# Optimization experiments

Hardware: AMD Instinct MI355X
Metric: run time of the kernel (lower is better)

## Reference

```python
import jax, jax.numpy as jnp
import numpy as np

N_NODES = 50000
N_EDGES = 800000
IN_SIZE = 128
NUM_HEADS = 8
HEAD_DIM = IN_SIZE // NUM_HEADS  # qk/val head dim = 16


def setup_inputs() -> dict:
    key = jax.random.key(0)
    ks = jax.random.split(key, 16)
    d = IN_SIZE
    lim = 1.0 / np.sqrt(d)
    inp = {
        "in_feats": jax.random.normal(ks[0], (N_NODES, d), jnp.float32),
        "struc_feats": jax.random.normal(ks[1], (N_NODES, d), jnp.float32),
        "edge_weights": jax.random.uniform(ks[2], (N_EDGES,), jnp.float32),
        "ln_scale": jnp.ones((d,), jnp.float32),
        "ln_bias": jnp.zeros((d,), jnp.float32),
        "Ws": jax.random.uniform(ks[3], (d, d), jnp.float32, -lim, lim),
        "bs": jnp.zeros((d,), jnp.float32),
        "Wq": jax.random.uniform(ks[4], (d, d), jnp.float32, -lim, lim),
        "bq": jnp.zeros((d,), jnp.float32),
        "Wk": jax.random.uniform(ks[5], (d, d), jnp.float32, -lim, lim),
        "bk": jnp.zeros((d,), jnp.float32),
        "Wv": jax.random.uniform(ks[6], (d, d), jnp.float32, -lim, lim),
        "bv": jnp.zeros((d,), jnp.float32),
        "Wo": jax.random.uniform(ks[7], (d, d), jnp.float32, -lim, lim),
        "edge_ids": jax.random.randint(ks[8], (2, N_EDGES), 0, N_NODES, jnp.int64)
        if jax.config.jax_enable_x64 else jax.random.randint(ks[8], (2, N_EDGES), 0, N_NODES, jnp.int32),
    }
    return inp


def _layer_norm(x, scale, bias, eps=1e-5):
    mu = jnp.mean(x, axis=-1, keepdims=True)
    var = jnp.var(x, axis=-1, keepdims=True)
    return (x - mu) * jax.lax.rsqrt(var + eps) * scale + bias


def reference(in_feats, struc_feats, edge_weights, ln_scale, ln_bias,
              Ws, bs, Wq, bq, Wk, bk, Wv, bv, Wo, edge_ids):
    N = in_feats.shape[0]
    H, hd = NUM_HEADS, HEAD_DIM

    delta = _layer_norm(in_feats, ln_scale, ln_bias)           # pre-norm
    delta = jax.nn.gelu(delta, approximate=False)               # pre-activation (exact GELU, torch default)
    delta_struc = delta + struc_feats @ Ws.T + bs               # struc_proj add

    qry = (delta_struc @ Wq.T + bq) / np.sqrt(hd)                # [N, qk]
    keyf = delta_struc @ Wk.T + bk                               # [N, qk]
    val = delta @ Wv.T + bv                                      # [N, val]

    src, dst = edge_ids[0], edge_ids[1]                          # out[src] += A[src,dst] * val[dst]
    qe = qry[src].reshape(-1, H, hd)                             # [E, H, hd]
    ke = keyf[dst].reshape(-1, H, hd)                            # [E, H, hd]
    attn = jax.nn.sigmoid(jnp.sum(qe * ke, axis=-1))             # [E, H]
    attn = edge_weights[:, None] * attn

    msgs = attn[:, :, None] * val[dst].reshape(-1, H, hd)        # [E, H, hd]
    agg = jax.ops.segment_sum(msgs.reshape(-1, H * hd), src, num_segments=N)  # [N, val]

    out = agg @ Wo.T                                             # out_proj (no bias)
    return in_feats + out                                        # skip connection
```

## Files before the change

### kernel.cpp

```cpp
#include <hip/hip_runtime.h>
#include <math.h>

#define NF 128

typedef __attribute__((ext_vector_type(8))) short short8;
typedef __attribute__((ext_vector_type(4))) float floatx4;

__device__ __forceinline__ unsigned short f2bf(float f) {
    union { float x; unsigned int i; } c; c.x = f;
    unsigned int r = c.i + 0x7fffu + ((c.i >> 16) & 1u);
    return (unsigned short)(r >> 16);
}
__device__ __forceinline__ float bf2f(unsigned short u) {
    union { unsigned int i; float x; } c; c.i = ((unsigned int)u) << 16;
    return c.x;
}
__device__ __forceinline__ void unpack8(uint4 u, float* f) {
    union { unsigned int i; float x; } c;
    c.i = u.x << 16;          f[0] = c.x;
    c.i = u.x & 0xffff0000u;  f[1] = c.x;
    c.i = u.y << 16;          f[2] = c.x;
    c.i = u.y & 0xffff0000u;  f[3] = c.x;
    c.i = u.z << 16;          f[4] = c.x;
    c.i = u.z & 0xffff0000u;  f[5] = c.x;
    c.i = u.w << 16;          f[6] = c.x;
    c.i = u.w & 0xffff0000u;  f[7] = c.x;
}
__device__ __forceinline__ ushort4 pack4(float a, float b, float c, float d) {
    ushort4 h; h.x = f2bf(a); h.y = f2bf(b); h.z = f2bf(c); h.w = f2bf(d);
    return h;
}

__global__ __launch_bounds__(256) void wconv5z_kernel(
    const float* __restrict__ a, const float* __restrict__ b,
    const float* __restrict__ c, const float* __restrict__ d,
    const float* __restrict__ e, unsigned short* __restrict__ o,
    int* __restrict__ cnt, int N)
{
    int blk = blockIdx.x;
    if (blk < 320) {
        int i = blk * 256 + threadIdx.x;
        int w = i >> 14, j = i & 16383;
        const float* p = (w == 0) ? a : (w == 1) ? b : (w == 2) ? c : (w == 3) ? d : e;
        o[i] = f2bf(p[j]);
    } else {
        int i = (blk - 320) * 256 + threadIdx.x;
        if (i < N) cnt[i] = 0;
    }
}

__global__ __launch_bounds__(256) void ln_kernel(
    const float* __restrict__ in_feats, const float* __restrict__ gamma,
    const float* __restrict__ beta, unsigned short* __restrict__ deltab, int M)
{
    int gi = blockIdx.x * 256 + threadIdx.x;
    int row = gi >> 2, t4 = gi & 3;
    if (row >= M) return;
    size_t rbase = (size_t)row * NF;

    const float4* ip = (const float4*)(in_feats + rbase) + t4 * 8;
    float4 xf[8];
    #pragma unroll
    for (int p = 0; p < 8; ++p) xf[p] = ip[p];
    float s = 0.f, sq = 0.f;
    #pragma unroll
    for (int p = 0; p < 8; ++p) {
        s  += xf[p].x + xf[p].y + xf[p].z + xf[p].w;
        sq += xf[p].x * xf[p].x + xf[p].y * xf[p].y
            + xf[p].z * xf[p].z + xf[p].w * xf[p].w;
    }
    s  += __shfl_xor(s, 1, 64);  s  += __shfl_xor(s, 2, 64);
    sq += __shfl_xor(sq, 1, 64); sq += __shfl_xor(sq, 2, 64);
    float mu = s * (1.0f / 128.0f);
    float var = sq * (1.0f / 128.0f) - mu * mu;
    float rstd = rsqrtf(var + 1e-5f);

    const float4* gp = (const float4*)gamma + t4 * 8;
    const float4* bp = (const float4*)beta + t4 * 8;
    uint dreg[16];
    #pragma unroll
    for (int p = 0; p < 8; ++p) {
        float4 g4 = gp[p], b4 = bp[p];
        float o0 = (xf[p].x - mu) * rstd * g4.x + b4.x;
        float o1 = (xf[p].y - mu) * rstd * g4.y + b4.y;
        float o2 = (xf[p].z - mu) * rstd * g4.z + b4.z;
        float o3 = (xf[p].w - mu) * rstd * g4.w + b4.w;
        o0 = 0.5f * o0 * (1.0f + erff(o0 * 0.70710678118654752f));
        o1 = 0.5f * o1 * (1.0f + erff(o1 * 0.70710678118654752f));
        o2 = 0.5f * o2 * (1.0f + erff(o2 * 0.70710678118654752f));
        o3 = 0.5f * o3 * (1.0f + erff(o3 * 0.70710678118654752f));
        ushort4 h = pack4(o0, o1, o2, o3);
        dreg[p * 2]     = (uint)h.x | ((uint)h.y << 16);
        dreg[p * 2 + 1] = (uint)h.z | ((uint)h.w << 16);
    }
    uint4* od = (uint4*)(deltab + rbase + t4 * 32);
    #pragma unroll
    for (int q = 0; q < 4; ++q)
        od[q] = make_uint4(dreg[q*4], dreg[q*4+1], dreg[q*4+2], dreg[q*4+3]);
}

__global__ __launch_bounds__(256) void gemm_dv_kernel(
    const float* __restrict__ struc, const unsigned short* __restrict__ deltab,
    const unsigned short* __restrict__ Wall, const float* __restrict__ bs,
    const float* __restrict__ bv, unsigned short* __restrict__ dstrb,
    unsigned short* __restrict__ kvb, int M, int nt)
{
    __shared__ unsigned short Wl[128][136];
    __shared__ unsigned short Cst[64][136];

    int tid = threadIdx.x;
    int y = blockIdx.y;
    int lane = tid & 63, w = tid >> 6, lg = lane & 15, quad = lane >> 4;

    const unsigned short* Wg = Wall + ((y == 0) ? 0 : 3 * 16384);
    const float* bias = (y == 0) ? bs : bv;
    unsigned short* outg = (y == 0) ? dstrb : (kvb + NF);
    int ostride = (y == 0) ? NF : 2 * NF;

    {
        const uint4* g = (const uint4*)Wg;
        #pragma unroll
        for (int p = 0; p < 8; ++p) {
            int idx = tid + p * 256;
            *(uint4*)&Wl[idx >> 4][(idx & 15) * 8] = g[idx];
        }
    }
    float br[8];
    #pragma unroll
    for (int t = 0; t < 8; ++t) br[t] = bias[t * 16 + lg];
    __syncthreads();

    for (int tile = blockIdx.x; tile < nt; tile += gridDim.x) {
        int m0 = tile * 64;
        int am = m0 + w * 16 + lg;
        size_t rb = (size_t)(am < M ? am : 0) * NF;

        short8 af[4];
        if (y == 0) {
            const float4* sp = (const float4*)(struc + rb);
            #pragma unroll
            for (int ks = 0; ks < 4; ++ks) {
                float4 f0 = sp[ks * 8 + quad * 2];
                float4 f1 = sp[ks * 8 + quad * 2 + 1];
                ushort4 h0 = pack4(f0.x, f0.y, f0.z, f0.w);
                ushort4 h1 = pack4(f1.x, f1.y, f1.z, f1.w);
                uint4 pk = make_uint4((uint)h0.x | ((uint)h0.y << 16),
                                      (uint)h0.z | ((uint)h0.w << 16),
                                      (uint)h1.x | ((uint)h1.y << 16),
                                      (uint)h1.z | ((uint)h1.w << 16));
                af[ks] = *(short8*)&pk;
            }
        } else {
            const unsigned short* arow = deltab + rb + quad * 8;
            #pragma unroll
            for (int ks = 0; ks < 4; ++ks) af[ks] = *(const short8*)(arow + ks * 32);
        }

        floatx4 acc[8];
        #pragma unroll
        for (int t = 0; t < 8; ++t) acc[t] = (floatx4){0.f, 0.f, 0.f, 0.f};
        #pragma unroll
        for (int ks = 0; ks < 4; ++ks) {
            #pragma unroll
            for (int t = 0; t < 8; ++t) {
                short8 b = *(const short8*)&Wl[t * 16 + lg][ks * 32 + quad * 8];
                acc[t] = __builtin_amdgcn_mfma_f32_16x16x32_bf16(af[ks], b, acc[t], 0, 0, 0);
            }
        }

        if (y == 0) {
            #pragma unroll
            for (int t = 0; t < 8; ++t) {
                int col = t * 16 + lg;
                #pragma unroll
                for (int r = 0; r < 4; ++r) {
                    int gm = m0 + w * 16 + quad * 4 + r;
                    float dadd = bf2f(deltab[(size_t)(gm < M ? gm : 0) * NF + col]);
                    Cst[w * 16 + quad * 4 + r][col] = f2bf(acc[t][r] + br[t] + dadd);
                }
            }
        } else {
            #pragma unroll
            for (int t = 0; t < 8; ++t) {
                int col = t * 16 + lg;
                #pragma unroll
                for (int r = 0; r < 4; ++r)
                    Cst[w * 16 + quad * 4 + r][col] = f2bf(acc[t][r] + br[t]);
            }
        }
        #pragma unroll
        for (int p = 0; p < 4; ++p) {
            int idx = lane + p * 64;
            int row = w * 16 + (idx >> 4), c16 = idx & 15;
            int gm = m0 + row;
            if (gm < M)
                *(uint4*)(outg + (size_t)gm * ostride + c16 * 8) = *(const uint4*)&Cst[row][c16 * 8];
        }
    }
}

__global__ __launch_bounds__(256) void gemm_qk_kernel(
    const unsigned short* __restrict__ dstrb, const unsigned short* __restrict__ Wall,
    const float* __restrict__ bq, const float* __restrict__ bk,
    unsigned short* __restrict__ qb, unsigned short* __restrict__ kvb,
    int M, int nt)
{
    __shared__ unsigned short Wl[128][136];
    __shared__ unsigned short Cst[64][136];

    int tid = threadIdx.x;
    int y = blockIdx.y;
    int lane = tid & 63, w = tid >> 6, lg = lane & 15, quad = lane >> 4;

    const unsigned short* Wg = Wall + (y + 1) * 16384;
    const float* bias = (y == 0) ? bq : bk;
    float scale = (y == 0) ? 0.25f : 1.0f;
    unsigned short* outg = (y == 0) ? qb : kvb;
    int ostride = (y == 0) ? NF : 2 * NF;

    {
        const uint4* g = (const uint4*)Wg;
        #pragma unroll
        for (int p = 0; p < 8; ++p) {
            int idx = tid + p * 256;
            *(uint4*)&Wl[idx >> 4][(idx & 15) * 8] = g[idx];
        }
    }
    float br[8];
    #pragma unroll
    for (int t = 0; t < 8; ++t) br[t] = bias[t * 16 + lg] * scale;
    __syncthreads();

    for (int tile = blockIdx.x; tile < nt; tile += gridDim.x) {
        int m0 = tile * 64;
        int am = m0 + w * 16 + lg;
        const unsigned short* arow = dstrb + (size_t)(am < M ? am : 0) * NF + quad * 8;

        floatx4 acc[8];
        #pragma unroll
        for (int t = 0; t < 8; ++t) acc[t] = (floatx4){0.f, 0.f, 0.f, 0.f};
        short8 af[4];
        #pragma unroll
        for (int ks = 0; ks < 4; ++ks) af[ks] = *(const short8*)(arow + ks * 32);
        #pragma unroll
        for (int ks = 0; ks < 4; ++ks) {
            #pragma unroll
            for (int t = 0; t < 8; ++t) {
                short8 b = *(const short8*)&Wl[t * 16 + lg][ks * 32 + quad * 8];
                acc[t] = __builtin_amdgcn_mfma_f32_16x16x32_bf16(af[ks], b, acc[t], 0, 0, 0);
            }
        }
        #pragma unroll
        for (int t = 0; t < 8; ++t) {
            int col = t * 16 + lg;
            #pragma unroll
            for (int r = 0; r < 4; ++r)
                Cst[w * 16 + quad * 4 + r][col] = f2bf(acc[t][r] * scale + br[t]);
        }
        #pragma unroll
        for (int p = 0; p < 4; ++p) {
            int idx = lane + p * 64;
            int row = w * 16 + (idx >> 4), c16 = idx & 15;
            int gm = m0 + row;
            if (gm < M)
                *(uint4*)(outg + (size_t)gm * ostride + c16 * 8) = *(const uint4*)&Cst[row][c16 * 8];
        }
    }
}

__global__ __launch_bounds__(256) void gemm_out_kernel(
    const unsigned short* __restrict__ Xb, const unsigned short* __restrict__ Wb,
    const float* __restrict__ addf, float* __restrict__ Y, int M, int nt)
{
    __shared__ unsigned short Wl[128][136];
    int tid = threadIdx.x;
    int lane = tid & 63, w = tid >> 6, lg = lane & 15, quad = lane >> 4;

    {
        const uint4* g = (const uint4*)Wb;
        #pragma unroll
        for (int p = 0; p < 8; ++p) {
            int idx = tid + p * 256;
            *(uint4*)&Wl[idx >> 4][(idx & 15) * 8] = g[idx];
        }
    }
    __syncthreads();

    for (int tile = blockIdx.x; tile < nt; tile += gridDim.x) {
        int m0 = tile * 64;
        int am = m0 + w * 16 + lg;
        const unsigned short* arow = Xb + (size_t)(am < M ? am : 0) * NF + quad * 8;

        floatx4 acc[8];
        #pragma unroll
        for (int t = 0; t < 8; ++t) acc[t] = (floatx4){0.f, 0.f, 0.f, 0.f};
        short8 af[4];
        #pragma unroll
        for (int ks = 0; ks < 4; ++ks) af[ks] = *(const short8*)(arow + ks * 32);
        #pragma unroll
        for (int ks = 0; ks < 4; ++ks) {
            #pragma unroll
            for (int t = 0; t < 8; ++t) {
                short8 b = *(const short8*)&Wl[t * 16 + lg][ks * 32 + quad * 8];
                acc[t] = __builtin_amdgcn_mfma_f32_16x16x32_bf16(af[ks], b, acc[t], 0, 0, 0);
            }
        }
        #pragma unroll
        for (int t = 0; t < 8; ++t) {
            int col = t * 16 + lg;
            #pragma unroll
            for (int r = 0; r < 4; ++r) {
                int gm = m0 + w * 16 + quad * 4 + r;
                if (gm >= M) continue;
                size_t off = (size_t)gm * NF + col;
                Y[off] = acc[t][r] + addf[off];
            }
        }
    }
}

__global__ void hist_kernel(const int* __restrict__ eid, int* __restrict__ cnt,
                            int* __restrict__ rank, int E)
{
    int i = blockIdx.x * blockDim.x + threadIdx.x;
    if (i < E) rank[i] = atomicAdd(&cnt[eid[i]], 1);
}

__global__ __launch_bounds__(256) void scan1_kernel(
    const int* __restrict__ cnt, int* __restrict__ bsum, int n)
{
    int base = blockIdx.x * 1024;
    int s = 0;
    #pragma unroll
    for (int p = 0; p < 4; ++p) {
        int i = base + (int)threadIdx.x + p * 256;
        if (i < n) s += cnt[i];
    }
    #pragma unroll
    for (int m = 1; m <= 32; m <<= 1) s += __shfl_xor(s, m, 64);
    __shared__ int ws_[4];
    int wid = threadIdx.x >> 6;
    if ((threadIdx.x & 63) == 0) ws_[wid] = s;
    __syncthreads();
    if (threadIdx.x == 0) bsum[blockIdx.x] = ws_[0] + ws_[1] + ws_[2] + ws_[3];
}

__global__ __launch_bounds__(256) void scan3_kernel(
    const int* __restrict__ cnt, const int* __restrict__ bsum,
    int* __restrict__ row_start, int n, int nb)
{
    __shared__ int base_off;
    int tid = threadIdx.x, lane = tid & 63, wid = tid >> 6;
    if (tid == 0) {
        int a = 0;
        for (int j = 0; j < (int)blockIdx.x; ++j) a += bsum[j];
        base_off = a;
        if ((int)blockIdx.x == nb - 1) {
            int tot = a;
            for (int j = blockIdx.x; j < nb; ++j) tot += bsum[j];
            row_start[n] = tot;
        }
    }
    int base = blockIdx.x * 1024;
    int v[4]; int s = 0;
    #pragma unroll
    for (int p = 0; p < 4; ++p) {
        int i = base + tid * 4 + p;
        v[p] = (i < n) ? cnt[i] : 0;
        s += v[p];
    }
    int ss = s;
    #pragma unroll
    for (int off = 1; off < 64; off <<= 1) {
        int t = __shfl_up(ss, off, 64);
        if (lane >= off) ss += t;
    }
    __shared__ int wsum[4];
    if (lane == 63) wsum[wid] = ss;
    __syncthreads();
    int woff = 0;
    for (int j = 0; j < wid; ++j) woff += wsum[j];
    int a = base_off + woff + (ss - s);
    #pragma unroll
    for (int p = 0; p < 4; ++p) {
        int i = base + tid * 4 + p;
        if (i < n) { row_start[i] = a; a += v[p]; }
    }
}

__global__ void scatter_kernel(const int* __restrict__ eid, const float* __restrict__ ew,
                               const int* __restrict__ row_start, const int* __restrict__ rank,
                               int2* __restrict__ edata, int E)
{
    int i = blockIdx.x * blockDim.x + threadIdx.x;
    if (i < E) {
        int src = eid[i];
        int pos = row_start[src] + rank[i];
        edata[pos] = make_int2(eid[E + i], __float_as_int(ew[i]));
    }
}

__global__ __launch_bounds__(256) void aggregate_kernel(
    const unsigned short* __restrict__ Q, const unsigned short* __restrict__ kvb,
    const int* __restrict__ row_start, const int2* __restrict__ edata,
    unsigned short* __restrict__ agg, int N)
{
    int node = blockIdx.x * 4 + (threadIdx.x >> 6);
    if (node >= N) return;
    int lane = threadIdx.x & 63;
    int sg = lane >> 4, lg = lane & 15;
    int rs = row_start[node], re = row_start[node + 1];

    float qv[8];
    unpack8(*(const uint4*)(Q + (size_t)node * NF + lg * 8), qv);
    float acc[8];
    #pragma unroll
    for (int j = 0; j < 8; ++j) acc[j] = 0.f;

    int e1 = rs + sg, e2 = rs + sg + 4;
    int2 ed1 = (e1 < re) ? edata[e1] : make_int2(0, 0);
    int2 ed2 = (e2 < re) ? edata[e2] : make_int2(0, 0);

    for (int e0 = rs; e0 < re; e0 += 8) {
        int2 c1 = ed1, c2 = ed2;
        int en1 = e0 + 8 + sg, en2 = en1 + 4;
        ed1 = (en1 < re) ? edata[en1] : make_int2(0, 0);
        ed2 = (en2 < re) ? edata[en2] : make_int2(0, 0);

        const uint4* p1 = (const uint4*)kvb + (size_t)c1.x * 32 + lg;
        const uint4* p2 = (const uint4*)kvb + (size_t)c2.x * 32 + lg;
        uint4 k1u = p1[0], v1u = p1[16];
        uint4 k2u = p2[0], v2u = p2[16];

        float kv1[8], kv2[8];
        unpack8(k1u, kv1);
        unpack8(k2u, kv2);
        float s1 = qv[0] * kv1[0], s2 = qv[0] * kv2[0];
        #pragma unroll
        for (int j = 1; j < 8; ++j) {
            s1 = fmaf(qv[j], kv1[j], s1);
            s2 = fmaf(qv[j], kv2[j], s2);
        }
        s1 += __shfl_xor(s1, 1, 64);
        s2 += __shfl_xor(s2, 1, 64);
        float a1 = __int_as_float(c1.y) / (1.f + __expf(-s1));
        float a2 = __int_as_float(c2.y) / (1.f + __expf(-s2));

        float vv1[8], vv2[8];
        unpack8(v1u, vv1);
        unpack8(v2u, vv2);
        #pragma unroll
        for (int j = 0; j < 8; ++j) {
            acc[j] = fmaf(a1, vv1[j], acc[j]);
            acc[j] = fmaf(a2, vv2[j], acc[j]);
        }
    }
    #pragma unroll
    for (int j = 0; j < 8; ++j) {
        acc[j] += __shfl_xor(acc[j], 16, 64);
        acc[j] += __shfl_xor(acc[j], 32, 64);
    }
    if (sg == 0) {
        unsigned short* o = agg + (size_t)node * NF + lg * 8;
        *(ushort4*)o       = pack4(acc[0], acc[1], acc[2], acc[3]);
        *(ushort4*)(o + 4) = pack4(acc[4], acc[5], acc[6], acc[7]);
    }
}

extern "C" void kernel_launch(void* const* d_in, const int* in_sizes, int n_in,
                              void* d_out, int out_size, void* d_ws, size_t ws_size,
                              hipStream_t stream)
{
    const float* in_feats = (const float*)d_in[0];
    const float* struc    = (const float*)d_in[1];
    const float* eweights = (const float*)d_in[2];
    const float* ln_scale = (const float*)d_in[3];
    const float* ln_bias  = (const float*)d_in[4];
    const float* Ws       = (const float*)d_in[5];
    const float* bs       = (const float*)d_in[6];
    const float* Wq       = (const float*)d_in[7];
    const float* bq       = (const float*)d_in[8];
    const float* Wk       = (const float*)d_in[9];
    const float* bk       = (const float*)d_in[10];
    const float* Wv       = (const float*)d_in[11];
    const float* bv       = (const float*)d_in[12];
    const float* Wo       = (const float*)d_in[13];
    const int*   edge_ids = (const int*)d_in[14];
    float* out = (float*)d_out;

    int N = in_sizes[0] / NF;
    int E = in_sizes[2];

    size_t F = (size_t)N * NF;
    unsigned short* deltab = (unsigned short*)d_ws;
    unsigned short* dstrb  = deltab + F;
    unsigned short* qb     = dstrb + F;
    unsigned short* kvb    = qb + F;
    unsigned short* aggb   = kvb + 2 * F;
    unsigned short* Wall   = aggb + F;
    int2*  edata     = (int2*)(Wall + 5 * 16384);
    int*   cnt       = (int*)(edata + E);
    int*   row_start = cnt + N;
    int*   bsum      = row_start + N + 1;
    int*   rank      = bsum + 64;

    int nt  = (N + 63) / 64;
    int geb = (E + 255) / 256;
    int nb  = (N + 1023) / 1024;
    int zb  = (N + 255) / 256;
    int lnb = (N * 4 + 255) / 256;

    wconv5z_kernel<<<320 + zb, 256, 0, stream>>>(Ws, Wq, Wk, Wv, Wo, Wall, cnt, N);

    hist_kernel<<<geb, 256, 0, stream>>>(edge_ids, cnt, rank, E);
    scan1_kernel<<<nb, 256, 0, stream>>>(cnt, bsum, N);
    scan3_kernel<<<nb, 256, 0, stream>>>(cnt, bsum, row_start, N, nb);
    scatter_kernel<<<geb, 256, 0, stream>>>(edge_ids, eweights, row_start, rank, edata, E);

    ln_kernel<<<lnb, 256, 0, stream>>>(in_feats, ln_scale, ln_bias, deltab, N);
    gemm_dv_kernel<<<dim3(261, 2), 256, 0, stream>>>(struc, deltab, Wall,
                                                     bs, bv, dstrb, kvb, N, nt);
    gemm_qk_kernel<<<dim3(261, 2), 256, 0, stream>>>(dstrb, Wall, bq, bk,
                                                     qb, kvb, N, nt);

    aggregate_kernel<<<(N + 3) / 4, 256, 0, stream>>>(qb, kvb, row_start, edata, aggb, N);

    gemm_out_kernel<<<nt, 256, 0, stream>>>(aggb, Wall + 4 * 16384, in_feats, out, N, nt);
}
```

Measured before the change: 294.7 us.

## Fold struc projection into composed Q/K weights and fuse QKV GEMMs

Precomputes Wq·Ws and Wk·Ws (plus the composed biases) in a small kernel. Q and K then come directly from delta and struc_feats as two accumulated MFMA products, so the intermediate delta_struc tensor and the dependent second GEMM pass are no longer needed. The Q, K and V projections run in one launch split across three outputs and two column halves. A prep kernel now converts struc to bf16 alongside the layernorm. The cost is extra MFMA work for Q and K, an extra bf16 struc buffer, and a different bf16 rounding path through the composed weights.

```diff
diff --git a/kernel.cpp b/kernel.cpp
--- a/kernel.cpp
+++ b/kernel.cpp
@@ -49,85 +49,143 @@
     }
 }
 
-__global__ __launch_bounds__(256) void ln_kernel(
-    const float* __restrict__ in_feats, const float* __restrict__ gamma,
-    const float* __restrict__ beta, unsigned short* __restrict__ deltab, int M)
+__global__ __launch_bounds__(256) void compose_kernel(
+    const float* __restrict__ Wq, const float* __restrict__ Wk,
+    const float* __restrict__ Ws, const float* __restrict__ bq,
+    const float* __restrict__ bk, const float* __restrict__ bs,
+    unsigned short* __restrict__ Wcomp, float* __restrict__ bias2)
+{
+    int id = blockIdx.x * 256 + threadIdx.x;
+    if (id < 32768) {
+        int m = id >> 14;
+        int rem = id & 16383;
+        int c = rem >> 7, j = rem & 127;
+        const float* W = m ? Wk : Wq;
+        float acc = 0.f;
+        #pragma unroll 4
+        for (int i = 0; i < 128; ++i)
+            acc = fmaf(W[c * 128 + i], Ws[i * 128 + j], acc);
+        Wcomp[id] = f2bf(acc);
+    } else if (id < 33024) {
+        int t = id - 32768;
+        int m = t >> 7, c = t & 127;
+        const float* W = m ? Wk : Wq;
+        const float* b = m ? bk : bq;
+        float acc = b[c];
+        for (int k = 0; k < 128; ++k) acc = fmaf(W[c * 128 + k], bs[k], acc);
+        bias2[m * 128 + c] = acc;
+    }
+}
+
+__global__ __launch_bounds__(256) void prep_kernel(
+    const float* __restrict__ in_feats, const float* __restrict__ struc,
+    const float* __restrict__ gamma, const float* __restrict__ beta,
+    unsigned short* __restrict__ deltab, unsigned short* __restrict__ strucb, int M)
 {
     int gi = blockIdx.x * 256 + threadIdx.x;
-    int row = gi >> 2, t4 = gi & 3;
+    int half = (gi >= M * 4) ? 1 : 0;
+    int li = half ? (gi - M * 4) : gi;
+    int row = li >> 2, t4 = li & 3;
     if (row >= M) return;
     size_t rbase = (size_t)row * NF;
 
-    const float4* ip = (const float4*)(in_feats + rbase) + t4 * 8;
-    float4 xf[8];
-    #pragma unroll
-    for (int p = 0; p < 8; ++p) xf[p] = ip[p];
-    float s = 0.f, sq = 0.f;
-    #pragma unroll
-    for (int p = 0; p < 8; ++p) {
-        s  += xf[p].x + xf[p].y + xf[p].z + xf[p].w;
-        sq += xf[p].x * xf[p].x + xf[p].y * xf[p].y
-            + xf[p].z * xf[p].z + xf[p].w * xf[p].w;
-    }
-    s  += __shfl_xor(s, 1, 64);  s  += __shfl_xor(s, 2, 64);
-    sq += __shfl_xor(sq, 1, 64); sq += __shfl_xor(sq, 2, 64);
-    float mu = s * (1.0f / 128.0f);
-    float var = sq * (1.0f / 128.0f) - mu * mu;
-    float rstd = rsqrtf(var + 1e-5f);
-
-    const float4* gp = (const float4*)gamma + t4 * 8;
-    const float4* bp = (const float4*)beta + t4 * 8;
-    uint dreg[16];
-    #pragma unroll
-    for (int p = 0; p < 8; ++p) {
-        float4 g4 = gp[p], b4 = bp[p];
-        float o0 = (xf[p].x - mu) * rstd * g4.x + b4.x;
-        float o1 = (xf[p].y - mu) * rstd * g4.y + b4.y;
-        float o2 = (xf[p].z - mu) * rstd * g4.z + b4.z;
-        float o3 = (xf[p].w - mu) * rstd * g4.w + b4.w;
-        o0 = 0.5f * o0 * (1.0f + erff(o0 * 0.70710678118654752f));
-        o1 = 0.5f * o1 * (1.0f + erff(o1 * 0.70710678118654752f));
-        o2 = 0.5f * o2 * (1.0f + erff(o2 * 0.70710678118654752f));
-        o3 = 0.5f * o3 * (1.0f + erff(o3 * 0.70710678118654752f));
-        ushort4 h = pack4(o0, o1, o2, o3);
-        dreg[p * 2]     = (uint)h.x | ((uint)h.y << 16);
-        dreg[p * 2 + 1] = (uint)h.z | ((uint)h.w << 16);
-    }
-    uint4* od = (uint4*)(deltab + rbase + t4 * 32);
-    #pragma unroll
-    for (int q = 0; q < 4; ++q)
-        od[q] = make_uint4(dreg[q*4], dreg[q*4+1], dreg[q*4+2], dreg[q*4+3]);
-}
-
-__global__ __launch_bounds__(256) void gemm_dv_kernel(
-    const float* __restrict__ struc, const unsigned short* __restrict__ deltab,
-    const unsigned short* __restrict__ Wall, const float* __restrict__ bs,
-    const float* __restrict__ bv, unsigned short* __restrict__ dstrb,
-    unsigned short* __restrict__ kvb, int M, int nt)
-{
-    __shared__ unsigned short Wl[128][136];
-    __shared__ unsigned short Cst[64][136];
+    if (!half) {
+        const float4* ip = (const float4*)(in_feats + rbase) + t4 * 8;
+        float4 xf[8];
+        #pragma unroll
+        for (int p = 0; p < 8; ++p) xf[p] = ip[p];
+        float s = 0.f, sq = 0.f;
+        #pragma unroll
+        for (int p = 0; p < 8; ++p) {
+            s  += xf[p].x + xf[p].y + xf[p].z + xf[p].w;
+            sq += xf[p].x * xf[p].x + xf[p].y * xf[p].y
+                + xf[p].z * xf[p].z + xf[p].w * xf[p].w;
+        }
+        s  += __shfl_xor(s, 1, 64);  s  += __shfl_xor(s, 2, 64);
+        sq += __shfl_xor(sq, 1, 64); sq += __shfl_xor(sq, 2, 64);
+        float mu = s * (1.0f / 128.0f);
+        float var = sq * (1.0f / 128.0f) - mu * mu;
+        float rstd = rsqrtf(var + 1e-5f);
+        const float4* gp = (const float4*)gamma + t4 * 8;
+        const float4* bp = (const float4*)beta + t4 * 8;
+        uint dreg[16];
+        #pragma unroll
+        for (int p = 0; p < 8; ++p) {
+            float4 g4 = gp[p], b4 = bp[p];
+            float o0 = (xf[p].x - mu) * rstd * g4.x + b4.x;
+            float o1 = (xf[p].y - mu) * rstd * g4.y + b4.y;
+            float o2 = (xf[p].z - mu) * rstd * g4.z + b4.z;
+            float o3 = (xf[p].w - mu) * rstd * g4.w + b4.w;
+            o0 = 0.5f * o0 * (1.0f + erff(o0 * 0.70710678118654752f));
+            o1 = 0.5f * o1 * (1.0f + erff(o1 * 0.70710678118654752f));
+            o2 = 0.5f * o2 * (1.0f + erff(o2 * 0.70710678118654752f));
+            o3 = 0.5f * o3 * (1.0f + erff(o3 * 0.70710678118654752f));
+            ushort4 h = pack4(o0, o1, o2, o3);
+            dreg[p * 2]     = (uint)h.x | ((uint)h.y << 16);
+            dreg[p * 2 + 1] = (uint)h.z | ((uint)h.w << 16);
+        }
+        uint4* od = (uint4*)(deltab + rbase + t4 * 32);
+        #pragma unroll
+        for (int q = 0; q < 4; ++q)
+            od[q] = make_uint4(dreg[q*4], dreg[q*4+1], dreg[q*4+2], dreg[q*4+3]);
+    } else {
+        const float4* sp = (const float4*)(struc + rbase) + t4 * 8;
+        uint4* od = (uint4*)(strucb + rbase + t4 * 32);
+        #pragma unroll
+        for (int p = 0; p < 4; ++p) {
+            float4 f0 = sp[p * 2], f1 = sp[p * 2 + 1];
+            ushort4 h0 = pack4(f0.x, f0.y, f0.z, f0.w);
+            ushort4 h1 = pack4(f1.x, f1.y, f1.z, f1.w);
+            od[p] = make_uint4((uint)h0.x | ((uint)h0.y << 16),
+                               (uint)h0.z | ((uint)h0.w << 16),
+                               (uint)h1.x | ((uint)h1.y << 16),
+                               (uint)h1.z | ((uint)h1.w << 16));
+        }
+    }
+}
+
+__global__ __launch_bounds__(256) void gemm_qkv_kernel(
+    const unsigned short* __restrict__ deltab, const unsigned short* __restrict__ strucb,
+    const unsigned short* __restrict__ Wall, const unsigned short* __restrict__ Wcomp,
+    const float* __restrict__ bias2, const float* __restrict__ bv,
+    unsigned short* __restrict__ qb, unsigned short* __restrict__ kvb,
+    int M, int nt)
+{
+    __shared__ unsigned short Wl[64][136];
+    __shared__ unsigned short W2[64][136];
+    __shared__ unsigned short Cst[64][72];
 
     int tid = threadIdx.x;
     int y = blockIdx.y;
+    int z = blockIdx.z;
+    int c0 = z * 64;
     int lane = tid & 63, w = tid >> 6, lg = lane & 15, quad = lane >> 4;
 
-    const unsigned short* Wg = Wall + ((y == 0) ? 0 : 3 * 16384);
-    const float* bias = (y == 0) ? bs : bv;
-    unsigned short* outg = (y == 0) ? dstrb : (kvb + NF);
+    const unsigned short* Wg = Wall + (y + 1) * 16384 + c0 * 128;
+    const float* bias = (y == 0) ? bias2 : (y == 1) ? (bias2 + 128) : bv;
+    float scale = (y == 0) ? 0.25f : 1.0f;
+    unsigned short* outg = (y == 0) ? qb : (y == 1) ? kvb : (kvb + NF);
     int ostride = (y == 0) ? NF : 2 * NF;
 
     {
         const uint4* g = (const uint4*)Wg;
         #pragma unroll
-        for (int p = 0; p < 8; ++p) {
+        for (int p = 0; p < 4; ++p) {
             int idx = tid + p * 256;
             *(uint4*)&Wl[idx >> 4][(idx & 15) * 8] = g[idx];
         }
-    }
-    float br[8];
-    #pragma unroll
-    for (int t = 0; t < 8; ++t) br[t] = bias[t * 16 + lg];
+        if (y < 2) {
+            const uint4* g2 = (const uint4*)(Wcomp + y * 16384 + c0 * 128);
+            #pragma unroll
+            for (int p = 0; p < 4; ++p) {
+                int idx = tid + p * 256;
+                *(uint4*)&W2[idx >> 4][(idx & 15) * 8] = g2[idx];
+            }
+        }
+    }
+    float br[4];
+    #pragma unroll
+    for (int t = 0; t < 4; ++t) br[t] = bias[c0 + t * 16 + lg] * scale;
     __syncthreads();
 
     for (int tile = blockIdx.x; tile < nt; tile += gridDim.x) {
@@ -135,135 +193,52 @@
         int am = m0 + w * 16 + lg;
         size_t rb = (size_t)(am < M ? am : 0) * NF;
 
-        short8 af[4];
-        if (y == 0) {
-            const float4* sp = (const float4*)(struc + rb);
+        floatx4 acc[4];
+        #pragma unroll
+        for (int t = 0; t < 4; ++t) acc[t] = (floatx4){0.f, 0.f, 0.f, 0.f};
+
+        {
+            const unsigned short* arow = deltab + rb + quad * 8;
+            short8 a1[4];
+            #pragma unroll
+            for (int ks = 0; ks < 4; ++ks) a1[ks] = *(const short8*)(arow + ks * 32);
             #pragma unroll
             for (int ks = 0; ks < 4; ++ks) {
-                float4 f0 = sp[ks * 8 + quad * 2];
-                float4 f1 = sp[ks * 8 + quad * 2 + 1];
-                ushort4 h0 = pack4(f0.x, f0.y, f0.z, f0.w);
-                ushort4 h1 = pack4(f1.x, f1.y, f1.z, f1.w);
-                uint4 pk = make_uint4((uint)h0.x | ((uint)h0.y << 16),
-                                      (uint)h0.z | ((uint)h0.w << 16),
-                                      (uint)h1.x | ((uint)h1.y << 16),
-                                      (uint)h1.z | ((uint)h1.w << 16));
-                af[ks] = *(short8*)&pk;
-            }
-        } else {
-            const unsigned short* arow = deltab + rb + quad * 8;
-            #pragma unroll
-            for (int ks = 0; ks < 4; ++ks) af[ks] = *(const short8*)(arow + ks * 32);
-        }
-
-        floatx4 acc[8];
-        #pragma unroll
-        for (int t = 0; t < 8; ++t) acc[t] = (floatx4){0.f, 0.f, 0.f, 0.f};
-        #pragma unroll
-        for (int ks = 0; ks < 4; ++ks) {
-            #pragma unroll
-            for (int t = 0; t < 8; ++t) {
-                short8 b = *(const short8*)&Wl[t * 16 + lg][ks * 32 + quad * 8];
-                acc[t] = __builtin_amdgcn_mfma_f32_16x16x32_bf16(af[ks], b, acc[t], 0, 0, 0);
-            }
-        }
-
-        if (y == 0) {
-            #pragma unroll
-            for (int t = 0; t < 8; ++t) {
-                int col = t * 16 + lg;
                 #pragma unroll
-                for (int r = 0; r < 4; ++r) {
-                    int gm = m0 + w * 16 + quad * 4 + r;
-                    float dadd = bf2f(deltab[(size_t)(gm < M ? gm : 0) * NF + col]);
-                    Cst[w * 16 + quad * 4 + r][col] = f2bf(acc[t][r] + br[t] + dadd);
+                for (int t = 0; t < 4; ++t) {
+                    short8 b = *(const short8*)&Wl[t * 16 + lg][ks * 32 + quad * 8];
+                    acc[t] = __builtin_amdgcn_mfma_f32_16x16x32_bf16(a1[ks], b, acc[t], 0, 0, 0);
                 }
             }
-        } else {
-            #pragma unroll
-            for (int t = 0; t < 8; ++t) {
-                int col = t * 16 + lg;
+        }
+        if (y < 2) {
+            const unsigned short* arow = strucb + rb + quad * 8;
+            short8 a2[4];
+            #pragma unroll
+            for (int ks = 0; ks < 4; ++ks) a2[ks] = *(const short8*)(arow + ks * 32);
+            #pragma unroll
+            for (int ks = 0; ks < 4; ++ks) {
                 #pragma unroll
-                for (int r = 0; r < 4; ++r)
-                    Cst[w * 16 + quad * 4 + r][col] = f2bf(acc[t][r] + br[t]);
+                for (int t = 0; t < 4; ++t) {
+                    short8 b = *(const short8*)&W2[t * 16 + lg][ks * 32 + quad * 8];
+                    acc[t] = __builtin_amdgcn_mfma_f32_16x16x32_bf16(a2[ks], b, acc[t], 0, 0, 0);
+                }
             }
         }
         #pragma unroll
-        for (int p = 0; p < 4; ++p) {
+        for (int t = 0; t < 4; ++t) {
+            int col = t * 16 + lg;
+            #pragma unroll
+            for (int r = 0; r < 4; ++r)
+                Cst[w * 16 + quad * 4 + r][col] = f2bf(acc[t][r] * scale + br[t]);
+        }
+        #pragma unroll
+        for (int p = 0; p < 2; ++p) {
             int idx = lane + p * 64;
-            int row = w * 16 + (idx >> 4), c16 = idx & 15;
+            int row = w * 16 + (idx >> 3), c8 = idx & 7;
             int gm = m0 + row;
             if (gm < M)
-                *(uint4*)(outg + (size_t)gm * ostride + c16 * 8) = *(const uint4*)&Cst[row][c16 * 8];
-        }
-    }
-}
-
-__global__ __launch_bounds__(256) void gemm_qk_kernel(
-    const unsigned short* __restrict__ dstrb, const unsigned short* __restrict__ Wall,
-    const float* __restrict__ bq, const float* __restrict__ bk,
-    unsigned short* __restrict__ qb, unsigned short* __restrict__ kvb,
-    int M, int nt)
-{
-    __shared__ unsigned short Wl[128][136];
-    __shared__ unsigned short Cst[64][136];
-
-    int tid = threadIdx.x;
-    int y = blockIdx.y;
-    int lane = tid & 63, w = tid >> 6, lg = lane & 15, quad = lane >> 4;
-
-    const unsigned short* Wg = Wall + (y + 1) * 16384;
-    const float* bias = (y == 0) ? bq : bk;
-    float scale = (y == 0) ? 0.25f : 1.0f;
-    unsigned short* outg = (y == 0) ? qb : kvb;
-    int ostride = (y == 0) ? NF : 2 * NF;
-
-    {
-        const uint4* g = (const uint4*)Wg;
-        #pragma unroll
-        for (int p = 0; p < 8; ++p) {
-            int idx = tid + p * 256;
-            *(uint4*)&Wl[idx >> 4][(idx & 15) * 8] = g[idx];
-        }
-    }
-    float br[8];
-    #pragma unroll
-    for (int t = 0; t < 8; ++t) br[t] = bias[t * 16 + lg] * scale;
-    __syncthreads();
-
-    for (int tile = blockIdx.x; tile < nt; tile += gridDim.x) {
-        int m0 = tile * 64;
-        int am = m0 + w * 16 + lg;
-        const unsigned short* arow = dstrb + (size_t)(am < M ? am : 0) * NF + quad * 8;
-
-        floatx4 acc[8];
-        #pragma unroll
-        for (int t = 0; t < 8; ++t) acc[t] = (floatx4){0.f, 0.f, 0.f, 0.f};
-        short8 af[4];
-        #pragma unroll
-        for (int ks = 0; ks < 4; ++ks) af[ks] = *(const short8*)(arow + ks * 32);
-        #pragma unroll
-        for (int ks = 0; ks < 4; ++ks) {
-            #pragma unroll
-            for (int t = 0; t < 8; ++t) {
-                short8 b = *(const short8*)&Wl[t * 16 + lg][ks * 32 + quad * 8];
-                acc[t] = __builtin_amdgcn_mfma_f32_16x16x32_bf16(af[ks], b, acc[t], 0, 0, 0);
-            }
-        }
-        #pragma unroll
-        for (int t = 0; t < 8; ++t) {
-            int col = t * 16 + lg;
-            #pragma unroll
-            for (int r = 0; r < 4; ++r)
-                Cst[w * 16 + quad * 4 + r][col] = f2bf(acc[t][r] * scale + br[t]);
-        }
-        #pragma unroll
-        for (int p = 0; p < 4; ++p) {
-            int idx = lane + p * 64;
-            int row = w * 16 + (idx >> 4), c16 = idx & 15;
-            int gm = m0 + row;
-            if (gm < M)
-                *(uint4*)(outg + (size_t)gm * ostride + c16 * 8) = *(const uint4*)&Cst[row][c16 * 8];
+                *(uint4*)(outg + (size_t)gm * ostride + c0 + c8 * 8) = *(const uint4*)&Cst[row][c8 * 8];
         }
     }
 }
@@ -493,12 +468,14 @@
 
     size_t F = (size_t)N * NF;
     unsigned short* deltab = (unsigned short*)d_ws;
-    unsigned short* dstrb  = deltab + F;
-    unsigned short* qb     = dstrb + F;
+    unsigned short* strucb = deltab + F;
+    unsigned short* qb     = strucb + F;
     unsigned short* kvb    = qb + F;
     unsigned short* aggb   = kvb + 2 * F;
     unsigned short* Wall   = aggb + F;
-    int2*  edata     = (int2*)(Wall + 5 * 16384);
+    unsigned short* Wcomp  = Wall + 5 * 16384;
+    float* bias2     = (float*)(Wcomp + 2 * 16384);
+    int2*  edata     = (int2*)(bias2 + 256);
     int*   cnt       = (int*)(edata + E);
     int*   row_start = cnt + N;
     int*   bsum      = row_start + N + 1;
@@ -508,20 +485,20 @@
     int geb = (E + 255) / 256;
     int nb  = (N + 1023) / 1024;
     int zb  = (N + 255) / 256;
-    int lnb = (N * 4 + 255) / 256;
+    int ppb = (8 * N + 255) / 256;
 
     wconv5z_kernel<<<320 + zb, 256, 0, stream>>>(Ws, Wq, Wk, Wv, Wo, Wall, cnt, N);
+    compose_kernel<<<129, 256, 0, stream>>>(Wq, Wk, Ws, bq, bk, bs, Wcomp, bias2);
 
     hist_kernel<<<geb, 256, 0, stream>>>(edge_ids, cnt, rank, E);
     scan1_kernel<<<nb, 256, 0, stream>>>(cnt, bsum, N);
     scan3_kernel<<<nb, 256, 0, stream>>>(cnt, bsum, row_start, N, nb);
     scatter_kernel<<<geb, 256, 0, stream>>>(edge_ids, eweights, row_start, rank, edata, E);
 
-    ln_kernel<<<lnb, 256, 0, stream>>>(in_feats, ln_scale, ln_bias, deltab, N);
-    gemm_dv_kernel<<<dim3(261, 2), 256, 0, stream>>>(struc, deltab, Wall,
-                                                     bs, bv, dstrb, kvb, N, nt);
-    gemm_qk_kernel<<<dim3(261, 2), 256, 0, stream>>>(dstrb, Wall, bq, bk,
-                                                     qb, kvb, N, nt);
+    prep_kernel<<<ppb, 256, 0, stream>>>(in_feats, struc, ln_scale, ln_bias,
+                                         deltab, strucb, N);
+    gemm_qkv_kernel<<<dim3(261, 3, 2), 256, 0, stream>>>(deltab, strucb, Wall, Wcomp,
+                                                         bias2, bv, qb, kvb, N, nt);
 
     aggregate_kernel<<<(N + 3) / 4, 256, 0, stream>>>(qb, kvb, row_start, edata, aggb, N);
 
```

Result: slower. 313.1 us (+6.2%).
